# Kernel tuning notes

Measured on AMD Instinct MI355X. Metric: run time of the kernel, lower is better.

The kernel has to match this reference:

```python
import jax, jax.numpy as jnp
import numpy as np

OSC_TIME = 10
UNITS = 256
D_IN = 256
BATCH = 32
SEQLEN = 2000


def setup_inputs() -> dict:
    key = jax.random.key(0)
    k1, k2, k3 = jax.random.split(key, 3)
    scale = 1.0 / np.sqrt(UNITS)
    x = jax.random.normal(k1, (BATCH, SEQLEN, D_IN), dtype=jnp.float32)
    W_x = jax.random.normal(k2, (4, 2, D_IN, UNITS), dtype=jnp.float32) * scale
    W_h = jax.random.normal(k3, (4, 2, UNITS, UNITS), dtype=jnp.float32) * scale
    b_x = jnp.zeros((4, 2, UNITS), dtype=jnp.float32)
    b_h = jnp.zeros((4, 2, UNITS), dtype=jnp.float32)
    return {"x": x, "W_x": W_x, "b_x": b_x, "W_h": W_h, "b_h": b_h}


def reference(x, W_x, b_x, W_h, b_h):
    # Subsample every OSC_TIME steps (tf.gather stride)
    xs = x[:, ::OSC_TIME]                       # [B, Ts, D]
    B, Ts, _ = xs.shape
    U = W_h.shape[-1]

    # Precompute input projections for all 4 cells x 2 gates: [4,2,B,Ts,U]
    xp = jnp.einsum('btd,cgdu->cgbtu', xs, W_x) + b_x[:, :, None, None, :]

    h0 = jnp.zeros((4, B, U), dtype=x.dtype)

    def ff_step(h, xp_t):                       # h [4,B,U], xp_t [4,2,B,U]
        hp = jnp.einsum('cbu,cguv->cgbv', h, W_h) + b_h[:, :, None, :]
        g = jax.nn.sigmoid(xp_t + hp)           # [4,2,B,U]
        j, k = g[:, 0], g[:, 1]
        h_new = j * (1.0 - h) + (1.0 - k) * h   # flip-flop update
        return h_new, h_new

    _, hs = jax.lax.scan(ff_step, h0, jnp.moveaxis(xp, 3, 0))  # hs [Ts,4,B,U]
    phi, omega, r, mu = hs[:, 0], hs[:, 1], hs[:, 2], hs[:, 3]  # each [Ts,B,U]

    # Oscillator: emit z = r*cos(phi) then update r, phi; OSC_TIME sub-steps
    def osc_step(carry, _):
        r_t, phi_t = carry
        z = r_t * jnp.cos(phi_t)
        r_n = r_t + (mu - jnp.square(r_t)) * r_t
        phi_n = phi_t + omega
        return (r_n, phi_n), z

    _, zs = jax.lax.scan(osc_step, (r, phi), None, length=OSC_TIME)  # [S,Ts,B,U]
    out = jnp.transpose(zs, (2, 1, 0, 3)).reshape(B, Ts * OSC_TIME, U)
    return out
```

## Files before the change

kernel.cpp:

```cpp
#include <hip/hip_runtime.h>
#include <hip/hip_fp16.h>
#include <stdint.h>

#define TS 200

typedef _Float16 h2_t  __attribute__((ext_vector_type(2)));
typedef _Float16 f16x8 __attribute__((ext_vector_type(8)));
typedef float    f32x4 __attribute__((ext_vector_type(4)));

static __device__ __forceinline__ float fdot2f(uint32_t w, uint32_t h, float acc) {
#if __has_builtin(__builtin_amdgcn_fdot2)
    return __builtin_amdgcn_fdot2(__builtin_bit_cast(h2_t, w),
                                  __builtin_bit_cast(h2_t, h), acc, false);
#else
    h2_t a = __builtin_bit_cast(h2_t, w), b = __builtin_bit_cast(h2_t, h);
    acc = fmaf((float)a.x, (float)b.x, acc);
    acc = fmaf((float)a.y, (float)b.y, acc);
    return acc;
#endif
}

template <int CTRL>
static __device__ __forceinline__ float dpp_add(float x) {
    int m = __builtin_amdgcn_update_dpp(0, __builtin_bit_cast(int, x), CTRL, 0xF, 0xF, true);
    return x + __builtin_bit_cast(float, m);
}
template <int CTRL>
static __device__ __forceinline__ float dpp_mov(float x) {
    int m = __builtin_amdgcn_update_dpp(0, __builtin_bit_cast(int, x), CTRL, 0xF, 0xF, true);
    return __builtin_bit_cast(float, m);
}

__global__ __launch_bounds__(256) void pack_all(const float* __restrict__ x,
                                                const float* __restrict__ Wx,
                                                const float* __restrict__ Wh,
                                                _Float16* __restrict__ xh,
                                                _Float16* __restrict__ wxt,
                                                uint32_t* __restrict__ wp) {
    int bid = blockIdx.x, tid = threadIdx.x;
    if (bid < 6400) {
        int row = bid, col = tid;
        int b = row / 200, t = row - b * 200;
        xh[(size_t)row * 256 + col] = (_Float16)x[((size_t)(b * 2000 + t * 10)) * 256 + col];
    } else if (bid < 8448) {
        int n = bid - 6400, k = tid;
        wxt[(size_t)n * 256 + k] = (_Float16)Wx[((size_t)((n >> 8) * 256 + k)) * 256 + (n & 255)];
    } else {
        int idx = (bid - 8448) * 256 + tid;
        int e   = idx & 3;
        int thr = (idx >> 2) & 1023;
        int j   = (idx >> 12) & 15;
        int c   = idx >> 16;
        int a = j >> 2, i = j & 3;
        int uu = a >> 1, g = a & 1;
        int vs = thr & 7, uq = (thr >> 3) & 7, wv = thr >> 6;
        int u = (wv * 8 + uq) * 2 + uu;
        int v = vs * 32 + i * 8 + e * 2;
        const float* base = Wh + ((size_t)((c * 2 + g) * 256 + v)) * 256 + u;
        h2_t p; p.x = (_Float16)base[0]; p.y = (_Float16)base[256];
        wp[idx] = __builtin_bit_cast(uint32_t, p);
    }
}

__global__ __launch_bounds__(256) void xp_gemm(const _Float16* __restrict__ xh,
                                               const _Float16* __restrict__ wxt,
                                               const float* __restrict__ bxf,
                                               _Float16* __restrict__ xp) {
    __shared__ _Float16 As[128 * 64];
    __shared__ _Float16 Bs[128 * 64];
    const int tid = threadIdx.x;
    const int lane = tid & 63, w = tid >> 6;
    const int m0 = (blockIdx.x >> 4) * 128;
    const int n0 = (blockIdx.x & 15) * 128;
    const int mw = (w & 1) * 64, nw = (w >> 1) * 64;

    f32x4 acc[4][4] = {};

    for (int kb = 0; kb < 4; kb++) {
        const int k0 = kb * 64;
#pragma unroll
        for (int q = 0; q < 4; q++) {
            int ii = w * 4 + q;
            int r = ii * 8 + (lane >> 3);
            int kcol = (lane & 7) * 8;
            const _Float16* ga = xh  + (size_t)(m0 + r) * 256 + k0 + kcol;
            const _Float16* gb = wxt + (size_t)(n0 + r) * 256 + k0 + kcol;
            __builtin_amdgcn_global_load_lds(
                (const __attribute__((address_space(1))) uint32_t*)ga,
                (__attribute__((address_space(3))) uint32_t*)(As + ii * 512), 16, 0, 0);
            __builtin_amdgcn_global_load_lds(
                (const __attribute__((address_space(1))) uint32_t*)gb,
                (__attribute__((address_space(3))) uint32_t*)(Bs + ii * 512), 16, 0, 0);
        }
        __syncthreads();
#pragma unroll
        for (int kc = 0; kc < 2; kc++) {
            f16x8 a[4], b[4];
#pragma unroll
            for (int mt = 0; mt < 4; mt++)
                a[mt] = *(const f16x8*)&As[(mw + mt * 16 + (lane & 15)) * 64 + kc * 32 + (lane >> 4) * 8];
#pragma unroll
            for (int nt = 0; nt < 4; nt++)
                b[nt] = *(const f16x8*)&Bs[(nw + nt * 16 + (lane & 15)) * 64 + kc * 32 + (lane >> 4) * 8];
#pragma unroll
            for (int mt = 0; mt < 4; mt++)
#pragma unroll
                for (int nt = 0; nt < 4; nt++)
                    acc[mt][nt] = __builtin_amdgcn_mfma_f32_16x16x32_f16(a[mt], b[nt], acc[mt][nt], 0, 0, 0);
        }
        __syncthreads();
    }

    const int nl = lane & 15, quad = lane >> 4;
#pragma unroll
    for (int nt = 0; nt < 4; nt++) {
        int n = n0 + nw + nt * 16 + nl;
        float bias = bxf[n];
        int c = n >> 9, gu = n & 511;
#pragma unroll
        for (int mt = 0; mt < 4; mt++)
#pragma unroll
            for (int r = 0; r < 4; r++) {
                int m = m0 + mw + mt * 16 + quad * 4 + r;
                int b = m / 200, t = m - b * 200;
                xp[((size_t)((c * 32 + b) * 200 + t)) * 512 + gu] =
                    (_Float16)(acc[mt][nt][r] + bias);
            }
    }
}

#define D4(ACC, W, H)                 \
    ACC = fdot2f(W.x, H.x, ACC);      \
    ACC = fdot2f(W.y, H.y, ACC);      \
    ACC = fdot2f(W.z, H.z, ACC);      \
    ACC = fdot2f(W.w, H.w, ACC);

#define PIN4(W) asm volatile("" : "+v"(W.x), "+v"(W.y), "+v"(W.z), "+v"(W.w))

#define LDS_BARRIER()                                        \
    do {                                                     \
        __builtin_amdgcn_sched_barrier(0);                   \
        asm volatile("s_waitcnt lgkmcnt(0)" ::: "memory");   \
        __builtin_amdgcn_s_barrier();                        \
        __builtin_amdgcn_sched_barrier(0);                   \
    } while (0)

__global__ __attribute__((amdgpu_flat_work_group_size(512, 512),
                          amdgpu_waves_per_eu(2, 2)))
void recurrence(const _Float16* __restrict__ xp,
                const float* __restrict__ bh,
                const uint32_t* __restrict__ Wp,
                float* __restrict__ hs) {
    const int cb  = blockIdx.x;
    const int c   = cb >> 5;
    const int tid = threadIdx.x;
    const int lane = tid & 63;
    const int vs = lane & 7;
    const int uq = lane >> 3;
    const int wv = tid >> 6;
    const int up0 = wv * 8 + uq;
    const int u0 = up0 * 2;

    __shared__ __align__(16) uint32_t h2s[2][160];

    const uint4* wb = (const uint4*)Wp + (size_t)c * 16 * 1024 + tid;
    uint4 wA00 = wb[0 * 1024],        wA01 = wb[1 * 1024],        wA02 = wb[2 * 1024],        wA03 = wb[3 * 1024];
    uint4 wA10 = wb[4 * 1024],        wA11 = wb[5 * 1024],        wA12 = wb[6 * 1024],        wA13 = wb[7 * 1024];
    uint4 wA20 = wb[8 * 1024],        wA21 = wb[9 * 1024],        wA22 = wb[10 * 1024],       wA23 = wb[11 * 1024];
    uint4 wA30 = wb[12 * 1024],       wA31 = wb[13 * 1024],       wA32 = wb[14 * 1024],       wA33 = wb[15 * 1024];
    uint4 wB00 = wb[0 * 1024 + 512],  wB01 = wb[1 * 1024 + 512],  wB02 = wb[2 * 1024 + 512],  wB03 = wb[3 * 1024 + 512];
    uint4 wB10 = wb[4 * 1024 + 512],  wB11 = wb[5 * 1024 + 512],  wB12 = wb[6 * 1024 + 512],  wB13 = wb[7 * 1024 + 512];
    uint4 wB20 = wb[8 * 1024 + 512],  wB21 = wb[9 * 1024 + 512],  wB22 = wb[10 * 1024 + 512], wB23 = wb[11 * 1024 + 512];
    uint4 wB30 = wb[12 * 1024 + 512], wB31 = wb[13 * 1024 + 512], wB32 = wb[14 * 1024 + 512], wB33 = wb[15 * 1024 + 512];
    PIN4(wA00); PIN4(wA01); PIN4(wA02); PIN4(wA03);
    PIN4(wA10); PIN4(wA11); PIN4(wA12); PIN4(wA13);
    PIN4(wA20); PIN4(wA21); PIN4(wA22); PIN4(wA23);
    PIN4(wA30); PIN4(wA31); PIN4(wA32); PIN4(wA33);
    PIN4(wB00); PIN4(wB01); PIN4(wB02); PIN4(wB03);
    PIN4(wB10); PIN4(wB11); PIN4(wB12); PIN4(wB13);
    PIN4(wB20); PIN4(wB21); PIN4(wB22); PIN4(wB23);
    PIN4(wB30); PIN4(wB31); PIN4(wB32); PIN4(wB33);

    float biasA = 0.f, biasB = 0.f;
    const _Float16* xpb = nullptr;
    if (vs < 4) {
        int g_sel = vs & 1, u_sel = u0 + (vs >> 1);
        biasA = bh[(c * 2 + g_sel) * 256 + u_sel];
        biasB = bh[(c * 2 + g_sel) * 256 + u_sel + 128];
        xpb  = xp + (size_t)cb * 200 * 512 + g_sel * 256 + u_sel;
    }

    float hregA = 0.f, hregB = 0.f;
    if (tid < 160) { h2s[0][tid] = 0u; }
    __syncthreads();

    float* hsb = hs + (size_t)cb * 200 * 256 + u0;

    _Float16 curA[8] = {}, curB[8] = {}, nxtA[8] = {}, nxtB[8] = {};
    if (vs < 4) {
#pragma unroll
        for (int s = 0; s < 8; s++) {
            curA[s] = xpb[(size_t)s * 512];
            curB[s] = xpb[(size_t)s * 512 + 128];
        }
    }

    for (int tb = 0; tb < TS; tb += 8) {
        if (vs < 4 && tb + 8 < TS) {
#pragma unroll
            for (int s = 0; s < 8; s++) {
                nxtA[s] = xpb[(size_t)(tb + 8 + s) * 512];
                nxtB[s] = xpb[(size_t)(tb + 8 + s) * 512 + 128];
            }
        }
#pragma unroll
        for (int s = 0; s < 8; s++) {
            const int t = tb + s;
            const uint32_t* hbuf = h2s[t & 1];
            uint32_t* hnext = h2s[(t + 1) & 1];

            float xpA = 0.f, xpB = 0.f;
            if (vs < 4) {
                xpA = (float)curA[s];
                xpB = (float)curB[s];
            }

            uint4 h0 = *(const uint4*)(hbuf + vs * 20 + 0);
            uint4 h1 = *(const uint4*)(hbuf + vs * 20 + 4);
            uint4 h2 = *(const uint4*)(hbuf + vs * 20 + 8);
            uint4 h3 = *(const uint4*)(hbuf + vs * 20 + 12);

            float aA0 = 0.f, aA1 = 0.f, aA2 = 0.f, aA3 = 0.f;
            float aB0 = 0.f, aB1 = 0.f, aB2 = 0.f, aB3 = 0.f;
            D4(aA0, wA00, h0) D4(aB0, wB00, h0) D4(aA1, wA10, h0) D4(aB1, wB10, h0)
            D4(aA2, wA20, h0) D4(aB2, wB20, h0) D4(aA3, wA30, h0) D4(aB3, wB30, h0)
            D4(aA0, wA01, h1) D4(aB0, wB01, h1) D4(aA1, wA11, h1) D4(aB1, wB11, h1)
            D4(aA2, wA21, h1) D4(aB2, wB21, h1) D4(aA3, wA31, h1) D4(aB3, wB31, h1)
            D4(aA0, wA02, h2) D4(aB0, wB02, h2) D4(aA1, wA12, h2) D4(aB1, wB12, h2)
            D4(aA2, wA22, h2) D4(aB2, wB22, h2) D4(aA3, wA32, h2) D4(aB3, wB32, h2)
            D4(aA0, wA03, h3) D4(aB0, wB03, h3) D4(aA1, wA13, h3) D4(aB1, wB13, h3)
            D4(aA2, wA23, h3) D4(aB2, wB23, h3) D4(aA3, wA33, h3) D4(aB3, wB33, h3)

            aA0 = dpp_add<0x141>(dpp_add<0x4E>(dpp_add<0xB1>(aA0)));
            aA1 = dpp_add<0x141>(dpp_add<0x4E>(dpp_add<0xB1>(aA1)));
            aA2 = dpp_add<0x141>(dpp_add<0x4E>(dpp_add<0xB1>(aA2)));
            aA3 = dpp_add<0x141>(dpp_add<0x4E>(dpp_add<0xB1>(aA3)));
            aB0 = dpp_add<0x141>(dpp_add<0x4E>(dpp_add<0xB1>(aB0)));
            aB1 = dpp_add<0x141>(dpp_add<0x4E>(dpp_add<0xB1>(aB1)));
            aB2 = dpp_add<0x141>(dpp_add<0x4E>(dpp_add<0xB1>(aB2)));
            aB3 = dpp_add<0x141>(dpp_add<0x4E>(dpp_add<0xB1>(aB3)));

            float sA = (vs == 0) ? aA0 : (vs == 1) ? aA1 : (vs == 2) ? aA2 : aA3;
            float sB = (vs == 0) ? aB0 : (vs == 1) ? aB1 : (vs == 2) ? aB2 : aB3;
            sA += xpA + biasA;
            sB += xpB + biasB;
            float sigA = 1.f / (1.f + __expf(-sA));
            float sigB = 1.f / (1.f + __expf(-sB));
            float kgA = dpp_mov<0xB1>(sigA);
            float kgB = dpp_mov<0xB1>(sigB);
            float hnA = sigA + hregA * (1.f - sigA - kgA);
            float hnB = sigB + hregB * (1.f - sigB - kgB);
            hregA = hnA;
            hregB = hnB;
            float hn1A = dpp_mov<0x4E>(hnA);
            float hn1B = dpp_mov<0x4E>(hnB);
            if (vs == 0) {
                h2_t pA; pA.x = (_Float16)hnA; pA.y = (_Float16)hn1A;
                h2_t pB; pB.x = (_Float16)hnB; pB.y = (_Float16)hn1B;
                int idx0 = (up0 >> 4) * 20 + (up0 & 15);
                hnext[idx0]      = __builtin_bit_cast(uint32_t, pA);
                hnext[idx0 + 80] = __builtin_bit_cast(uint32_t, pB);
                *(float2*)(hsb + (size_t)t * 256)       = make_float2(hnA, hn1A);
                *(float2*)(hsb + (size_t)t * 256 + 128) = make_float2(hnB, hn1B);
            }
            LDS_BARRIER();
        }
        if (vs < 4) {
#pragma unroll
            for (int s = 0; s < 8; s++) { curA[s] = nxtA[s]; curB[s] = nxtB[s]; }
        }
    }
}

__global__ __launch_bounds__(256) void osc(const float* __restrict__ hs,
                                           float* __restrict__ out) {
    int tid = blockIdx.x * 256 + threadIdx.x;
    const int cstride = 32 * 200 * 256;
    int u = tid & 255;
    int bt = tid >> 8;
    int t = bt % 200, b = bt / 200;
    float phi   = hs[0 * cstride + tid];
    float omega = hs[1 * cstride + tid];
    float r     = hs[2 * cstride + tid];
    float mu    = hs[3 * cstride + tid];
    float* o = out + ((size_t)(b * 2000 + t * 10)) * 256 + u;
#pragma unroll
    for (int s = 0; s < 10; s++) {
        o[(size_t)s * 256] = r * __cosf(phi);
        r = r + (mu - r * r) * r;
        phi = phi + omega;
    }
}

extern "C" void kernel_launch(void* const* d_in, const int* in_sizes, int n_in,
                              void* d_out, int out_size, void* d_ws, size_t ws_size,
                              hipStream_t stream) {
    const float* x  = (const float*)d_in[0];
    const float* Wx = (const float*)d_in[1];
    const float* bx = (const float*)d_in[2];
    const float* Wh = (const float*)d_in[3];
    const float* bh = (const float*)d_in[4];
    float* out = (float*)d_out;

    char* ws = (char*)d_ws;
    const size_t XP = (size_t)4 * 32 * 200 * 512 * 2;
    const size_t HS = (size_t)4 * 32 * 200 * 256 * 4;
    const size_t XH = (size_t)6400 * 256 * 2;

    _Float16* xp  = (_Float16*)ws;
    float*    hs  = (float*)(ws + XP);
    _Float16* xh  = (_Float16*)(ws + XP);
    _Float16* wxt = (_Float16*)(ws + XP + XH);
    uint32_t* wp  = (uint32_t*)(ws + XP + HS);

    pack_all<<<9472, 256, 0, stream>>>(x, Wx, Wh, xh, wxt, wp);
    xp_gemm<<<800, 256, 0, stream>>>(xh, wxt, bx, xp);
    recurrence<<<128, 512, 0, stream>>>(xp, bh, wp, hs);
    osc<<<6400, 256, 0, stream>>>(hs, out);
}
```

Measured before the change: 344.9 us.

## Replace per-step workgroup barrier with LDS flag spin-wait and triple buffering

Swaps the s_barrier after every recurrence step for per-wave progress flags in LDS. Each wave publishes its step count once its h writes land and spins until all eight waves reach the current step. A third h buffer keeps a fast wave from overwriting a buffer that slower waves are still reading, so waves can drift up to one step apart. Spinning on volatile LDS loads costs issue slots and LDS bandwidth, and correctness depends on LDS write ordering across waves.

Measured after the change: 392.8 us. +13.9%, slower.

```diff
diff --git a/kernel.cpp b/kernel.cpp
--- a/kernel.cpp
+++ b/kernel.cpp
@@ -137,14 +137,6 @@
 
 #define PIN4(W) asm volatile("" : "+v"(W.x), "+v"(W.y), "+v"(W.z), "+v"(W.w))
 
-#define LDS_BARRIER()                                        \
-    do {                                                     \
-        __builtin_amdgcn_sched_barrier(0);                   \
-        asm volatile("s_waitcnt lgkmcnt(0)" ::: "memory");   \
-        __builtin_amdgcn_s_barrier();                        \
-        __builtin_amdgcn_sched_barrier(0);                   \
-    } while (0)
-
 __global__ __attribute__((amdgpu_flat_work_group_size(512, 512),
                           amdgpu_waves_per_eu(2, 2)))
 void recurrence(const _Float16* __restrict__ xp,
@@ -161,7 +153,8 @@
     const int up0 = wv * 8 + uq;
     const int u0 = up0 * 2;
 
-    __shared__ __align__(16) uint32_t h2s[2][160];
+    __shared__ __align__(16) uint32_t h2s[3][160];
+    __shared__ uint32_t Fw[8];
 
     const uint4* wb = (const uint4*)Wp + (size_t)c * 16 * 1024 + tid;
     uint4 wA00 = wb[0 * 1024],        wA01 = wb[1 * 1024],        wA02 = wb[2 * 1024],        wA03 = wb[3 * 1024];
@@ -192,9 +185,14 @@
 
     float hregA = 0.f, hregB = 0.f;
     if (tid < 160) { h2s[0][tid] = 0u; }
+    if (tid >= 160 && tid < 168) { Fw[tid - 160] = 0u; }
     __syncthreads();
 
     float* hsb = hs + (size_t)cb * 200 * 256 + u0;
+
+    uint32_t* bR = h2s[0];
+    uint32_t* bW = h2s[1];
+    uint32_t* bS = h2s[2];
 
     _Float16 curA[8] = {}, curB[8] = {}, nxtA[8] = {}, nxtB[8] = {};
     if (vs < 4) {
@@ -216,8 +214,18 @@
 #pragma unroll
         for (int s = 0; s < 8; s++) {
             const int t = tb + s;
-            const uint32_t* hbuf = h2s[t & 1];
-            uint32_t* hnext = h2s[(t + 1) & 1];
+
+            {
+                volatile const uint32_t* Fv = (volatile const uint32_t*)Fw;
+                uint32_t mn;
+                do {
+                    uint32_t f0 = Fv[0], f1 = Fv[1], f2 = Fv[2], f3 = Fv[3];
+                    uint32_t f4 = Fv[4], f5 = Fv[5], f6 = Fv[6], f7 = Fv[7];
+                    mn = min(min(min(f0, f1), min(f2, f3)),
+                             min(min(f4, f5), min(f6, f7)));
+                } while (mn < (uint32_t)t);
+                __builtin_amdgcn_sched_barrier(0);
+            }
 
             float xpA = 0.f, xpB = 0.f;
             if (vs < 4) {
@@ -225,10 +233,10 @@
                 xpB = (float)curB[s];
             }
 
-            uint4 h0 = *(const uint4*)(hbuf + vs * 20 + 0);
-            uint4 h1 = *(const uint4*)(hbuf + vs * 20 + 4);
-            uint4 h2 = *(const uint4*)(hbuf + vs * 20 + 8);
-            uint4 h3 = *(const uint4*)(hbuf + vs * 20 + 12);
+            uint4 h0 = *(const uint4*)(bR + vs * 20 + 0);
+            uint4 h1 = *(const uint4*)(bR + vs * 20 + 4);
+            uint4 h2 = *(const uint4*)(bR + vs * 20 + 8);
+            uint4 h3 = *(const uint4*)(bR + vs * 20 + 12);
 
             float aA0 = 0.f, aA1 = 0.f, aA2 = 0.f, aA3 = 0.f;
             float aB0 = 0.f, aB1 = 0.f, aB2 = 0.f, aB3 = 0.f;
@@ -264,16 +272,26 @@
             hregB = hnB;
             float hn1A = dpp_mov<0x4E>(hnA);
             float hn1B = dpp_mov<0x4E>(hnB);
+            float2 stA = make_float2(hnA, hn1A);
+            float2 stB = make_float2(hnB, hn1B);
             if (vs == 0) {
                 h2_t pA; pA.x = (_Float16)hnA; pA.y = (_Float16)hn1A;
                 h2_t pB; pB.x = (_Float16)hnB; pB.y = (_Float16)hn1B;
                 int idx0 = (up0 >> 4) * 20 + (up0 & 15);
-                hnext[idx0]      = __builtin_bit_cast(uint32_t, pA);
-                hnext[idx0 + 80] = __builtin_bit_cast(uint32_t, pB);
-                *(float2*)(hsb + (size_t)t * 256)       = make_float2(hnA, hn1A);
-                *(float2*)(hsb + (size_t)t * 256 + 128) = make_float2(hnB, hn1B);
-            }
-            LDS_BARRIER();
+                bW[idx0]      = __builtin_bit_cast(uint32_t, pA);
+                bW[idx0 + 80] = __builtin_bit_cast(uint32_t, pB);
+            }
+            __builtin_amdgcn_sched_barrier(0);
+            asm volatile("s_waitcnt lgkmcnt(0)" ::: "memory");
+            if (lane == 0) {
+                *(volatile uint32_t*)&Fw[wv] = (uint32_t)(t + 1);
+            }
+            __builtin_amdgcn_sched_barrier(0);
+            if (vs == 0) {
+                *(float2*)(hsb + (size_t)t * 256)       = stA;
+                *(float2*)(hsb + (size_t)t * 256 + 128) = stB;
+            }
+            uint32_t* tmp = bR; bR = bW; bW = bS; bS = tmp;
         }
         if (vs < 4) {
 #pragma unroll
```
